# Optimization experiments

Measured on AMD Instinct MI355X. Metric: run time of the kernel, lower is better.

Reference implementation:

```python
import jax, jax.numpy as jnp
import numpy as np

B, S, H, L, NH, F, V = 8, 512, 768, 12, 12, 3072, 21128
DH = H // NH
SEP = 102
NEG = -1e9  # eager BERT additive mask: (1-mask)*large_negative


def _ln(x, g, b, eps=1e-12):
    m = jnp.mean(x, axis=-1, keepdims=True)
    v = jnp.var(x, axis=-1, keepdims=True)
    return (x - m) * jax.lax.rsqrt(v + eps) * g + b


def _mask_bias(input_ids):
    # prefix-LM mask: tokens <= first SEP fully bidirectional; suffix causal + sees prefix
    hit = input_ids == SEP                      # [B,S]
    has_sep = jnp.any(hit, axis=1)              # [B]
    first = jnp.argmax(hit, axis=1)             # [B] (first SEP position)
    sep = jnp.minimum(first, S - 2)             # clamp as in torch code
    pos = jnp.arange(S)
    i = pos[None, :, None]
    j = pos[None, None, :]
    sb = sep[:, None, None]
    vis = (j <= sb) | ((i > sb) & (j <= i))     # [B,S,S]
    vis = jnp.where(has_sep[:, None, None], vis, True)  # no SEP -> full ones
    return jnp.where(vis, 0.0, NEG).astype(jnp.float32)[:, None]  # [B,1,S,S]


def setup_inputs():
    key = jax.random.key(0)
    ks = jax.random.split(key, 4)
    input_ids = jax.random.randint(ks[0], (B, S), 0, V)
    sep_pos = jax.random.randint(ks[1], (B,), 32, 128)
    input_ids = input_ids.at[jnp.arange(B), sep_pos].set(SEP)
    labels = jax.random.randint(ks[2], (B, S), 0, V)
    pk = jax.random.split(ks[3], 10)
    n = lambda k, sh: jax.random.normal(k, sh, jnp.float32) * 0.02
    return dict(
        input_ids=input_ids, labels=labels,
        word_emb=n(pk[0], (V, H)), pos_emb=n(pk[1], (S, H)), type_emb=n(pk[2], (2, H)),
        emb_g=jnp.ones((H,), jnp.float32), emb_b=jnp.zeros((H,), jnp.float32),
        Wq=n(pk[3], (L, H, H)), bq=jnp.zeros((L, H), jnp.float32),
        Wk=n(pk[4], (L, H, H)), bk=jnp.zeros((L, H), jnp.float32),
        Wv=n(pk[5], (L, H, H)), bv=jnp.zeros((L, H), jnp.float32),
        Wo=n(pk[6], (L, H, H)), bo=jnp.zeros((L, H), jnp.float32),
        ln1_g=jnp.ones((L, H), jnp.float32), ln1_b=jnp.zeros((L, H), jnp.float32),
        W1=n(pk[7], (L, H, F)), b1=jnp.zeros((L, F), jnp.float32),
        W2=n(pk[8], (L, F, H)), b2=jnp.zeros((L, H), jnp.float32),
        ln2_g=jnp.ones((L, H), jnp.float32), ln2_b=jnp.zeros((L, H), jnp.float32),
        cls_W=n(pk[9], (H, V)), cls_b=jnp.zeros((V,), jnp.float32),
    )


def reference(input_ids, labels, word_emb, pos_emb, type_emb, emb_g, emb_b,
              Wq, bq, Wk, bk, Wv, bv, Wo, bo, ln1_g, ln1_b,
              W1, b1, W2, b2, ln2_g, ln2_b, cls_W, cls_b):
    bias = _mask_bias(input_ids)                               # [B,1,S,S]
    x = word_emb[input_ids] + pos_emb[None, :S] + type_emb[0]  # [B,S,H]
    x = _ln(x, emb_g, emb_b)

    def layer(h, p):
        wq, bq_, wk, bk_, wv, bv_, wo, bo_, g1, g1b, w1, bb1, w2, bb2, g2, g2b = p
        heads = lambda t: t.reshape(B, S, NH, DH).transpose(0, 2, 1, 3)
        q = heads(h @ wq + bq_)
        k = heads(h @ wk + bk_)
        v = heads(h @ wv + bv_)
        scores = jnp.einsum('bhqd,bhkd->bhqk', q, k) / np.sqrt(DH).astype(np.float32) + bias
        probs = jax.nn.softmax(scores, axis=-1)
        ctx = jnp.einsum('bhqk,bhkd->bhqd', probs, v).transpose(0, 2, 1, 3).reshape(B, S, H)
        h = _ln(h + ctx @ wo + bo_, g1, g1b)
        ffn = jax.nn.gelu(h @ w1 + bb1, approximate=False) @ w2 + bb2
        h = _ln(h + ffn, g2, g2b)
        return h, None

    x, _ = jax.lax.scan(layer, x, (Wq, bq, Wk, bk, Wv, bv, Wo, bo,
                                   ln1_g, ln1_b, W1, b1, W2, b2, ln2_g, ln2_b))
    logits = x @ cls_W + cls_b                                 # [B,S,V]

    # per-sample CE: mean over tokens after first SEP; full-sequence CE if no SEP
    logp = jax.nn.log_softmax(logits, axis=-1)
    ce = -jnp.take_along_axis(logp, labels[..., None], axis=-1)[..., 0]  # [B,S]
    hit = input_ids == SEP
    has_sep = jnp.any(hit, axis=1)
    first = jnp.argmax(hit, axis=1)
    pos = jnp.arange(S)[None]
    m = jnp.where(has_sep[:, None], pos > first[:, None], True).astype(ce.dtype)
    per_sample = jnp.sum(ce * m, axis=1) / jnp.sum(m, axis=1)
    return jnp.mean(per_sample)
```

## Files before the change

kernel.cpp:

```cpp
#include <hip/hip_runtime.h>
#include <math.h>

typedef unsigned short ushort;
typedef __bf16 bf16x8 __attribute__((ext_vector_type(8)));
typedef float f32x4 __attribute__((ext_vector_type(4)));

constexpr int Bb  = 8;
constexpr int Ss  = 512;
constexpr int Hh  = 768;
constexpr int Ll  = 12;
constexpr int NHh = 12;
constexpr int Ff  = 3072;
constexpr int Vv  = 21128;
constexpr int DHh = 64;
constexpr int Mm  = Bb * Ss;
constexpr int SEP_ID = 102;
constexpr int VP  = 21504;
constexpr int NCH = 24;
constexpr int TPC = 7;
constexpr int QKVN = 3 * Hh;
constexpr float LSE_SHIFT = 20.0f;

static __device__ __forceinline__ ushort f2bf(float f) {
    unsigned u = __float_as_uint(f);
    unsigned r = (u + 0x7fffu + ((u >> 16) & 1u)) >> 16;
    return (ushort)r;
}
static __device__ __forceinline__ float bf2f(unsigned x) {
    return __uint_as_float(x << 16);
}

__global__ __launch_bounds__(512) void sep_kernel(const int* __restrict__ ids,
                                                  int* __restrict__ info)
{
    int b = blockIdx.x;
    int t = threadIdx.x;
    int v = (ids[b * Ss + t] == SEP_ID) ? t : 0x7FFFFFFF;
    #pragma unroll
    for (int off = 32; off; off >>= 1) {
        int o = __shfl_xor(v, off);
        v = min(v, o);
    }
    __shared__ int wmin[8];
    int lane = t & 63, wid = t >> 6;
    if (lane == 0) wmin[wid] = v;
    __syncthreads();
    if (t == 0) {
        int first = wmin[0];
        #pragma unroll
        for (int w = 1; w < 8; w++) first = min(first, wmin[w]);
        int has = (first != 0x7FFFFFFF) ? 1 : 0;
        info[b * 4 + 0] = first;
        info[b * 4 + 1] = has;
        info[b * 4 + 2] = has ? min(first, Ss - 2) : (Ss + 1);
    }
}

__global__ __launch_bounds__(256) void embed_ln_kernel(
    const int* __restrict__ ids, const float* __restrict__ we,
    const float* __restrict__ pe, const float* __restrict__ te,
    const float* __restrict__ g, const float* __restrict__ bp,
    float* __restrict__ x, ushort* __restrict__ xb)
{
    int tok = blockIdx.x;
    int s = tok & (Ss - 1);
    int tid = threadIdx.x;
    int id = ids[tok];
    float e[3];
    #pragma unroll
    for (int r = 0; r < 3; r++) {
        int h = tid + (r << 8);
        e[r] = we[(size_t)id * Hh + h] + pe[(size_t)s * Hh + h] + te[h];
    }
    float sum = e[0] + e[1] + e[2];
    float sq  = fmaf(e[0], e[0], fmaf(e[1], e[1], e[2] * e[2]));
    #pragma unroll
    for (int off = 32; off; off >>= 1) {
        sum += __shfl_xor(sum, off);
        sq  += __shfl_xor(sq, off);
    }
    __shared__ float red[8];
    int lane = tid & 63, wid = tid >> 6;
    if (lane == 0) { red[wid] = sum; red[4 + wid] = sq; }
    __syncthreads();
    sum = red[0] + red[1] + red[2] + red[3];
    sq  = red[4] + red[5] + red[6] + red[7];
    float mean = sum * (1.0f / Hh);
    float var  = sq * (1.0f / Hh) - mean * mean;
    float rstd = rsqrtf(var + 1e-12f);
    #pragma unroll
    for (int r = 0; r < 3; r++) {
        int h = tid + (r << 8);
        float v = (e[r] - mean) * rstd * g[h] + bp[h];
        x[(size_t)tok * Hh + h] = v;
        xb[(size_t)tok * Hh + h] = f2bf(v);
    }
}

__global__ __launch_bounds__(256) void resid_ln_kernel(
    const float* __restrict__ resid, const float* __restrict__ y,
    const float* __restrict__ g, const float* __restrict__ bp,
    float* __restrict__ out, ushort* __restrict__ outb)
{
    int tok = blockIdx.x;
    int tid = threadIdx.x;
    float e[3];
    #pragma unroll
    for (int r = 0; r < 3; r++) {
        int h = tid + (r << 8);
        size_t idx = (size_t)tok * Hh + h;
        e[r] = resid[idx] + y[idx];
    }
    float sum = e[0] + e[1] + e[2];
    float sq  = fmaf(e[0], e[0], fmaf(e[1], e[1], e[2] * e[2]));
    #pragma unroll
    for (int off = 32; off; off >>= 1) {
        sum += __shfl_xor(sum, off);
        sq  += __shfl_xor(sq, off);
    }
    __shared__ float red[8];
    int lane = tid & 63, wid = tid >> 6;
    if (lane == 0) { red[wid] = sum; red[4 + wid] = sq; }
    __syncthreads();
    sum = red[0] + red[1] + red[2] + red[3];
    sq  = red[4] + red[5] + red[6] + red[7];
    float mean = sum * (1.0f / Hh);
    float var  = sq * (1.0f / Hh) - mean * mean;
    float rstd = rsqrtf(var + 1e-12f);
    #pragma unroll
    for (int r = 0; r < 3; r++) {
        int h = tid + (r << 8);
        float v = (e[r] - mean) * rstd * g[h] + bp[h];
        out[(size_t)tok * Hh + h] = v;
        outb[(size_t)tok * Hh + h] = f2bf(v);
    }
}

__global__ __launch_bounds__(256) void resid_ln4_kernel(
    const float* __restrict__ resid, const float* __restrict__ p,
    const float* __restrict__ bias, const float* __restrict__ g,
    const float* __restrict__ bp,
    float* __restrict__ out, ushort* __restrict__ outb)
{
    const size_t MHl = (size_t)Mm * Hh;
    int tok = blockIdx.x;
    int tid = threadIdx.x;
    float e[3];
    #pragma unroll
    for (int r = 0; r < 3; r++) {
        int h = tid + (r << 8);
        size_t idx = (size_t)tok * Hh + h;
        float acc = resid[idx] + bias[h];
        acc += p[idx];
        acc += p[MHl + idx];
        acc += p[2 * MHl + idx];
        acc += p[3 * MHl + idx];
        e[r] = acc;
    }
    float sum = e[0] + e[1] + e[2];
    float sq  = fmaf(e[0], e[0], fmaf(e[1], e[1], e[2] * e[2]));
    #pragma unroll
    for (int off = 32; off; off >>= 1) {
        sum += __shfl_xor(sum, off);
        sq  += __shfl_xor(sq, off);
    }
    __shared__ float red[8];
    int lane = tid & 63, wid = tid >> 6;
    if (lane == 0) { red[wid] = sum; red[4 + wid] = sq; }
    __syncthreads();
    sum = red[0] + red[1] + red[2] + red[3];
    sq  = red[4] + red[5] + red[6] + red[7];
    float mean = sum * (1.0f / Hh);
    float var  = sq * (1.0f / Hh) - mean * mean;
    float rstd = rsqrtf(var + 1e-12f);
    #pragma unroll
    for (int r = 0; r < 3; r++) {
        int h = tid + (r << 8);
        float v = (e[r] - mean) * rstd * g[h] + bp[h];
        out[(size_t)tok * Hh + h] = v;
        outb[(size_t)tok * Hh + h] = f2bf(v);
    }
}

__global__ __launch_bounds__(256) void prep_kernel(
    const float* __restrict__ Wq, const float* __restrict__ Wk,
    const float* __restrict__ Wv, const float* __restrict__ Wo,
    const float* __restrict__ W1, const float* __restrict__ W2,
    const float* __restrict__ bq, const float* __restrict__ bk,
    const float* __restrict__ bv,
    ushort* __restrict__ qkvoT, ushort* __restrict__ w1T,
    ushort* __restrict__ w2T, float* __restrict__ bqkv)
{
    int b = blockIdx.x;
    if (b >= 6912) {
        for (int j = threadIdx.x; j < Hh; j += 256) {
            bqkv[j]          = bq[j];
            bqkv[Hh + j]     = bk[j];
            bqkv[2 * Hh + j] = bv[j];
        }
        return;
    }
    const float* W;
    ushort* Wt;
    int K, N, n0, k0;
    if (b < 2304) {
        int which = b / 576, t = b % 576;
        const float* srcs[4] = { Wq, Wk, Wv, Wo };
        W = srcs[which];
        Wt = qkvoT + (size_t)which * Hh * Hh;
        K = Hh; N = Hh;
        n0 = (t % 24) * 32; k0 = (t / 24) * 32;
    } else if (b < 4608) {
        int t = b - 2304;
        W = W1; Wt = w1T; K = Hh; N = Ff;
        n0 = (t % 96) * 32; k0 = (t / 96) * 32;
    } else {
        int t = b - 4608;
        W = W2; Wt = w2T; K = Ff; N = Hh;
        n0 = (t % 24) * 32; k0 = (t / 24) * 32;
    }
    __shared__ float ts[32][33];
    int tx = threadIdx.x & 31, ty = threadIdx.x >> 5;
    #pragma unroll
    for (int i = 0; i < 32; i += 8)
        ts[ty + i][tx] = W[(size_t)(k0 + ty + i) * N + n0 + tx];
    __syncthreads();
    #pragma unroll
    for (int i = 0; i < 32; i += 8)
        Wt[(size_t)(n0 + ty + i) * K + k0 + tx] = f2bf(ts[tx][ty + i]);
}

__global__ __launch_bounds__(256) void pad_transpose_kernel(
    const float* __restrict__ W, ushort* __restrict__ Wt, int K, int N)
{
    __shared__ float ts[32][33];
    int n0 = blockIdx.x * 32, k0 = blockIdx.y * 32;
    int tx = threadIdx.x & 31, ty = threadIdx.x >> 5;
    #pragma unroll
    for (int i = 0; i < 32; i += 8) {
        int n = n0 + tx;
        ts[ty + i][tx] = (n < N) ? W[(size_t)(k0 + ty + i) * N + n] : 0.f;
    }
    __syncthreads();
    #pragma unroll
    for (int i = 0; i < 32; i += 8)
        Wt[(size_t)(n0 + ty + i) * K + k0 + tx] = f2bf(ts[tx][ty + i]);
}

__global__ __launch_bounds__(256) void bias_pad_kernel(
    const float* __restrict__ cb, float* __restrict__ cbp)
{
    int i = blockIdx.x * 256 + threadIdx.x;
    if (i < VP) cbp[i] = (i < Vv) ? cb[i] : -1.0e9f;
}

template <int ACT, int OUT_BF, int BIAS>
__global__ __launch_bounds__(256) void mfma_gemm(
    const ushort* __restrict__ A,
    const ushort* __restrict__ Bt,
    const float* __restrict__ bias,
    void* __restrict__ C,
    int N, int K, int lda, int ldb)
{
    __shared__ __align__(16) ushort As[128 * 32];
    __shared__ __align__(16) ushort Bs[128 * 32];
    const int tid = threadIdx.x;
    const int lane = tid & 63, wid = tid >> 6;
    const int m0 = blockIdx.y * 128, n0 = blockIdx.x * 128;
    const int kbase = blockIdx.z * K;
    const size_t zoff = (size_t)blockIdx.z * Mm * N;
    A += kbase;
    Bt += kbase;
    const int wr = (wid >> 1) * 64, wc = (wid & 1) * 64;
    const int lr = lane & 15;
    const int kg = (lane >> 4) << 3;

    f32x4 acc[4][4];
    #pragma unroll
    for (int mi = 0; mi < 4; ++mi)
        #pragma unroll
        for (int ni = 0; ni < 4; ++ni)
            acc[mi][ni] = (f32x4){0.f, 0.f, 0.f, 0.f};

    for (int k0 = 0; k0 < K; k0 += 32) {
        #pragma unroll
        for (int i = 0; i < 2; ++i) {
            int idx = i * 256 + tid;
            int r = idx >> 2, c = (idx & 3) << 3;
            __builtin_amdgcn_global_load_lds(
                (const __attribute__((address_space(1))) void*)(A + (size_t)(m0 + r) * lda + k0 + c),
                (__attribute__((address_space(3))) void*)(As + (size_t)(i * 256 + (wid << 6)) * 8),
                16, 0, 0);
        }
        #pragma unroll
        for (int i = 0; i < 2; ++i) {
            int idx = i * 256 + tid;
            int r = idx >> 2, c = (idx & 3) << 3;
            __builtin_amdgcn_global_load_lds(
                (const __attribute__((address_space(1))) void*)(Bt + (size_t)(n0 + r) * ldb + k0 + c),
                (__attribute__((address_space(3))) void*)(Bs + (size_t)(i * 256 + (wid << 6)) * 8),
                16, 0, 0);
        }
        __syncthreads();

        bf16x8 af[4], bfr[4];
        #pragma unroll
        for (int mi = 0; mi < 4; ++mi)
            af[mi] = *(const bf16x8*)(As + (size_t)(wr + mi * 16 + lr) * 32 + kg);
        #pragma unroll
        for (int ni = 0; ni < 4; ++ni)
            bfr[ni] = *(const bf16x8*)(Bs + (size_t)(wc + ni * 16 + lr) * 32 + kg);

        #pragma unroll
        for (int mi = 0; mi < 4; ++mi)
            #pragma unroll
            for (int ni = 0; ni < 4; ++ni)
                acc[mi][ni] = __builtin_amdgcn_mfma_f32_16x16x32_bf16(
                    af[mi], bfr[ni], acc[mi][ni], 0, 0, 0);
        __syncthreads();
    }

    #pragma unroll
    for (int ni = 0; ni < 4; ++ni) {
        int col = n0 + wc + ni * 16 + lr;
        float bsv = 0.f;
        if (BIAS) bsv = bias[col];
        #pragma unroll
        for (int mi = 0; mi < 4; ++mi) {
            f32x4 v = acc[mi][ni];
            #pragma unroll
            for (int q = 0; q < 4; ++q) {
                int row = m0 + wr + mi * 16 + ((lane >> 4) << 2) + q;
                float val = v[q] + bsv;
                if (ACT == 1) {
                    float y = 0.7978845608028654f
                              * (val + 0.044715f * val * val * val);
                    val = val / (1.0f + __expf(-2.0f * y));
                }
                if (OUT_BF)
                    ((ushort*)C)[(size_t)row * N + col] = f2bf(val);
                else
                    ((float*)C)[zoff + (size_t)row * N + col] = val;
            }
        }
    }
}

constexpr int SP = 65;
constexpr int PS = 72;
constexpr int VS = 72;

__global__ __launch_bounds__(256) void flash_attn_kernel(
    const ushort* __restrict__ qkv, const int* __restrict__ info,
    ushort* __restrict__ ctx)
{
    __shared__ __align__(16) ushort K_lds[64 * VS];
    __shared__ __align__(16) ushort Vt_lds[64 * VS];
    __shared__ __align__(16) ushort P_lds[64 * PS];
    __shared__ float S_lds[64 * SP];
    __shared__ float m_s[64], l_s[64], rf_s[64];

    const int tid = threadIdx.x;
    const int lane = tid & 63, wid = tid >> 6;
    const int bh = blockIdx.y, b = bh / NHh, h = bh % NHh;
    const int i0 = blockIdx.x * 64;
    const int lr = lane & 15, hi = lane >> 4;
    const int kg = hi << 3;
    const int wr = (wid >> 1) * 32;
    const int wc = (wid & 1) * 32;
    const int has = info[b * 4 + 1], sep = info[b * 4 + 2];
    const size_t tok0 = (size_t)b * Ss;

    bf16x8 qf[2][2];
    #pragma unroll
    for (int mi = 0; mi < 2; ++mi)
        #pragma unroll
        for (int kk = 0; kk < 2; ++kk)
            qf[mi][kk] = *(const bf16x8*)&qkv[(tok0 + i0 + wr + mi * 16 + lr) * QKVN
                                             + h * DHh + kk * 32 + kg];

    f32x4 o[2][2];
    #pragma unroll
    for (int mi = 0; mi < 2; ++mi)
        #pragma unroll
        for (int ni = 0; ni < 2; ++ni)
            o[mi][ni] = (f32x4){0.f, 0.f, 0.f, 0.f};

    if (tid < 64) { m_s[tid] = -3.0e38f; l_s[tid] = 0.f; }
    __syncthreads();

    for (int j0 = 0; j0 < Ss; j0 += 64) {
        #pragma unroll
        for (int i = 0; i < 2; ++i) {
            int ix = i * 256 + tid;
            int r = ix >> 3, c = (ix & 7) << 3;
            uint4 kq = *(const uint4*)&qkv[(tok0 + j0 + r) * QKVN + Hh + h * DHh + c];
            *(uint4*)&K_lds[(size_t)r * VS + c] = kq;
        }
        {
            int kv0 = (tid & 15) * 4;
            int d0 = (tid >> 4) * 4;
            uint2 rv[4];
            #pragma unroll
            for (int r = 0; r < 4; ++r)
                rv[r] = *(const uint2*)&qkv[(tok0 + j0 + kv0 + r) * QKVN
                                            + 2 * Hh + h * DHh + d0];
            #pragma unroll
            for (int c = 0; c < 4; ++c) {
                unsigned e0 = (c < 2) ? (rv[0].x >> (16 * c)) : (rv[0].y >> (16 * (c - 2)));
                unsigned e1 = (c < 2) ? (rv[1].x >> (16 * c)) : (rv[1].y >> (16 * (c - 2)));
                unsigned e2 = (c < 2) ? (rv[2].x >> (16 * c)) : (rv[2].y >> (16 * (c - 2)));
                unsigned e3 = (c < 2) ? (rv[3].x >> (16 * c)) : (rv[3].y >> (16 * (c - 2)));
                uint2 packed;
                packed.x = (e0 & 0xffffu) | (e1 << 16);
                packed.y = (e2 & 0xffffu) | (e3 << 16);
                *(uint2*)&Vt_lds[(size_t)(d0 + c) * VS + kv0] = packed;
            }
        }
        __syncthreads();

        f32x4 s[2][2];
        #pragma unroll
        for (int mi = 0; mi < 2; ++mi)
            #pragma unroll
            for (int ni = 0; ni < 2; ++ni)
                s[mi][ni] = (f32x4){0.f, 0.f, 0.f, 0.f};
        #pragma unroll
        for (int ni = 0; ni < 2; ++ni)
            #pragma unroll
            for (int kk = 0; kk < 2; ++kk) {
                bf16x8 kf = *(const bf16x8*)&K_lds[(size_t)(wc + ni * 16 + lr) * VS
                                                   + kk * 32 + kg];
                #pragma unroll
                for (int mi = 0; mi < 2; ++mi)
                    s[mi][ni] = __builtin_amdgcn_mfma_f32_16x16x32_bf16(
                        qf[mi][kk], kf, s[mi][ni], 0, 0, 0);
            }
        #pragma unroll
        for (int mi = 0; mi < 2; ++mi)
            #pragma unroll
            for (int ni = 0; ni < 2; ++ni)
                #pragma unroll
                for (int q = 0; q < 4; ++q) {
                    int rl = wr + mi * 16 + hi * 4 + q;
                    int cl = wc + ni * 16 + lr;
                    int gi = i0 + rl, gj = j0 + cl;
                    bool vis = (!has) || (gj <= sep) || ((gi > sep) && (gj <= gi));
                    S_lds[rl * SP + cl] = s[mi][ni][q] * 0.125f
                                          + (vis ? 0.0f : -1000000000.0f);
                }
        __syncthreads();

        {
            int r = tid >> 2, c0 = (tid & 3) * 16;
            float mold = m_s[r];
            float sv[16];
            float tmax = -3.0e38f;
            #pragma unroll
            for (int c = 0; c < 16; ++c) {
                sv[c] = S_lds[r * SP + c0 + c];
                tmax = fmaxf(tmax, sv[c]);
            }
            tmax = fmaxf(tmax, __shfl_xor(tmax, 1));
            tmax = fmaxf(tmax, __shfl_xor(tmax, 2));
            float mnew = fmaxf(mold, tmax);
            float sum = 0.f;
            #pragma unroll
            for (int c = 0; c < 16; ++c) {
                float p = __expf(sv[c] - mnew);
                P_lds[r * PS + c0 + c] = f2bf(p);
                sum += p;
            }
            sum += __shfl_xor(sum, 1);
            sum += __shfl_xor(sum, 2);
            if ((tid & 3) == 0) {
                float rf = __expf(mold - mnew);
                rf_s[r] = rf;
                l_s[r] = l_s[r] * rf + sum;
                m_s[r] = mnew;
            }
        }
        __syncthreads();

        #pragma unroll
        for (int mi = 0; mi < 2; ++mi)
            #pragma unroll
            for (int q = 0; q < 4; ++q) {
                float rf = rf_s[wr + mi * 16 + hi * 4 + q];
                #pragma unroll
                for (int ni = 0; ni < 2; ++ni)
                    o[mi][ni][q] *= rf;
            }
        #pragma unroll
        for (int kk = 0; kk < 2; ++kk) {
            bf16x8 pf[2];
            #pragma unroll
            for (int mi = 0; mi < 2; ++mi)
                pf[mi] = *(const bf16x8*)&P_lds[(size_t)(wr + mi * 16 + lr) * PS
                                                + kk * 32 + kg];
            #pragma unroll
            for (int ni = 0; ni < 2; ++ni) {
                bf16x8 vf = *(const bf16x8*)&Vt_lds[(size_t)(wc + ni * 16 + lr) * VS
                                                    + kk * 32 + kg];
                #pragma unroll
                for (int mi = 0; mi < 2; ++mi)
                    o[mi][ni] = __builtin_amdgcn_mfma_f32_16x16x32_bf16(
                        pf[mi], vf, o[mi][ni], 0, 0, 0);
            }
        }
        __syncthreads();
    }

    #pragma unroll
    for (int mi = 0; mi < 2; ++mi)
        #pragma unroll
        for (int q = 0; q < 4; ++q) {
            int rl = wr + mi * 16 + hi * 4 + q;
            float inv = 1.0f / l_s[rl];
            #pragma unroll
            for (int ni = 0; ni < 2; ++ni)
                ctx[(tok0 + i0 + rl) * Hh + h * DHh + wc + ni * 16 + lr]
                    = f2bf(o[mi][ni][q] * inv);
        }
}

__global__ __launch_bounds__(256) void cls_lse_kernel(
    const ushort* __restrict__ A,
    const ushort* __restrict__ WT,
    const float* __restrict__ cbp,
    const int* __restrict__ labels,
    float* __restrict__ psv, float* __restrict__ pll)
{
    __shared__ __align__(16) ushort As[128 * 32];
    __shared__ __align__(16) ushort Bs[128 * 32];
    __shared__ float ssum[2][128];
    __shared__ float sll[128];
    __shared__ int lab[128];
    const int tid = threadIdx.x;
    const int lane = tid & 63, wid = tid >> 6;
    const int m0 = blockIdx.y * 128;
    const int chunk = blockIdx.x;
    if (tid < 128) {
        sll[tid] = 0.f;
        lab[tid] = labels[m0 + tid];
    }
    const int wr = (wid >> 1) * 64, wcid = wid & 1, wc = wcid * 64;
    const int lr = lane & 15;
    const int hi = lane >> 4;
    const int kg = hi << 3;

    float sacc[16];
    #pragma unroll
    for (int i = 0; i < 16; ++i) sacc[i] = 0.f;

    for (int t = 0; t < TPC; ++t) {
        const int n0 = (chunk * TPC + t) * 128;
        f32x4 acc[4][4];
        #pragma unroll
        for (int mi = 0; mi < 4; ++mi)
            #pragma unroll
            for (int ni = 0; ni < 4; ++ni)
                acc[mi][ni] = (f32x4){0.f, 0.f, 0.f, 0.f};

        for (int k0 = 0; k0 < Hh; k0 += 32) {
            #pragma unroll
            for (int i = 0; i < 2; ++i) {
                int idx = i * 256 + tid;
                int r = idx >> 2, c = (idx & 3) << 3;
                __builtin_amdgcn_global_load_lds(
                    (const __attribute__((address_space(1))) void*)(A + (size_t)(m0 + r) * Hh + k0 + c),
                    (__attribute__((address_space(3))) void*)(As + (size_t)(i * 256 + (wid << 6)) * 8),
                    16, 0, 0);
            }
            #pragma unroll
            for (int i = 0; i < 2; ++i) {
                int idx = i * 256 + tid;
                int r = idx >> 2, c = (idx & 3) << 3;
                __builtin_amdgcn_global_load_lds(
                    (const __attribute__((address_space(1))) void*)(WT + (size_t)(n0 + r) * Hh + k0 + c),
                    (__attribute__((address_space(3))) void*)(Bs + (size_t)(i * 256 + (wid << 6)) * 8),
                    16, 0, 0);
            }
            __syncthreads();

            bf16x8 af[4], bfr[4];
            #pragma unroll
            for (int mi = 0; mi < 4; ++mi)
                af[mi] = *(const bf16x8*)(As + (size_t)(wr + mi * 16 + lr) * 32 + kg);
            #pragma unroll
            for (int ni = 0; ni < 4; ++ni)
                bfr[ni] = *(const bf16x8*)(Bs + (size_t)(wc + ni * 16 + lr) * 32 + kg);

            #pragma unroll
            for (int mi = 0; mi < 4; ++mi)
                #pragma unroll
                for (int ni = 0; ni < 4; ++ni)
                    acc[mi][ni] = __builtin_amdgcn_mfma_f32_16x16x32_bf16(
                        af[mi], bfr[ni], acc[mi][ni], 0, 0, 0);
            __syncthreads();
        }

        float bvs[4];
        int cols[4];
        #pragma unroll
        for (int ni = 0; ni < 4; ++ni) {
            cols[ni] = n0 + wc + ni * 16 + lr;
            bvs[ni] = cbp[cols[ni]];
        }
        #pragma unroll
        for (int mi = 0; mi < 4; ++mi) {
            #pragma unroll
            for (int q = 0; q < 4; ++q) {
                int rl = wr + mi * 16 + hi * 4 + q;
                float v0 = acc[mi][0][q] + bvs[0];
                float v1 = acc[mi][1][q] + bvs[1];
                float v2 = acc[mi][2][q] + bvs[2];
                float v3 = acc[mi][3][q] + bvs[3];
                int lb = lab[rl];
                if (lb == cols[0]) sll[rl] = v0;
                if (lb == cols[1]) sll[rl] = v1;
                if (lb == cols[2]) sll[rl] = v2;
                if (lb == cols[3]) sll[rl] = v3;
                sacc[mi * 4 + q] += __expf(v0 - LSE_SHIFT) + __expf(v1 - LSE_SHIFT)
                                  + __expf(v2 - LSE_SHIFT) + __expf(v3 - LSE_SHIFT);
            }
        }
    }

    #pragma unroll
    for (int mi = 0; mi < 4; ++mi) {
        #pragma unroll
        for (int q = 0; q < 4; ++q) {
            float s = sacc[mi * 4 + q];
            s += __shfl_xor(s, 1);
            s += __shfl_xor(s, 2);
            s += __shfl_xor(s, 4);
            s += __shfl_xor(s, 8);
            if (lr == 0) ssum[wcid][wr + mi * 16 + hi * 4 + q] = s;
        }
    }
    __syncthreads();
    if (tid < 128) {
        psv[(size_t)chunk * Mm + m0 + tid] = ssum[0][tid] + ssum[1][tid];
        pll[(size_t)chunk * Mm + m0 + tid] = sll[tid];
    }
}

__global__ __launch_bounds__(256) void cls_merge_kernel(
    const float* __restrict__ psv, const float* __restrict__ pll,
    float* __restrict__ ce)
{
    int row = blockIdx.x * 256 + threadIdx.x;
    float s = 0.f, l = 0.f;
    #pragma unroll 1
    for (int c = 0; c < NCH; ++c) {
        s += psv[(size_t)c * Mm + row];
        l += pll[(size_t)c * Mm + row];
    }
    ce[row] = (LSE_SHIFT + logf(s)) - l;
}

__global__ __launch_bounds__(256) void ce_reduce_kernel(
    const float* __restrict__ ce, const int* __restrict__ info,
    float* __restrict__ ps)
{
    int b = blockIdx.x, tid = threadIdx.x;
    int first = info[b * 4 + 0], has = info[b * 4 + 1];
    float sum = 0.0f;
    for (int s = tid; s < Ss; s += 256) {
        bool mv = has ? (s > first) : true;
        if (mv) sum += ce[b * Ss + s];
    }
    #pragma unroll
    for (int off = 32; off; off >>= 1) sum += __shfl_xor(sum, off);
    __shared__ float red[4];
    int lane = tid & 63, wid = tid >> 6;
    if (lane == 0) red[wid] = sum;
    __syncthreads();
    if (tid == 0) {
        float tot = red[0] + red[1] + red[2] + red[3];
        float cnt = has ? (float)(Ss - 1 - first) : (float)Ss;
        ps[b] = tot / cnt;
    }
}

__global__ void final_kernel(const float* __restrict__ ps, float* __restrict__ out)
{
    if (threadIdx.x == 0 && blockIdx.x == 0) {
        float t = 0.0f;
        #pragma unroll
        for (int b = 0; b < Bb; b++) t += ps[b];
        out[0] = t * (1.0f / Bb);
    }
}

extern "C" void kernel_launch(void* const* d_in, const int* in_sizes, int n_in,
                              void* d_out, int out_size, void* d_ws, size_t ws_size,
                              hipStream_t stream)
{
    const int*   ids    = (const int*)d_in[0];
    const int*   labels = (const int*)d_in[1];
    const float* we     = (const float*)d_in[2];
    const float* pe     = (const float*)d_in[3];
    const float* te     = (const float*)d_in[4];
    const float* eg     = (const float*)d_in[5];
    const float* ebp    = (const float*)d_in[6];
    const float* Wq     = (const float*)d_in[7];
    const float* bq     = (const float*)d_in[8];
    const float* Wk     = (const float*)d_in[9];
    const float* bk     = (const float*)d_in[10];
    const float* Wv     = (const float*)d_in[11];
    const float* bv     = (const float*)d_in[12];
    const float* Wo     = (const float*)d_in[13];
    const float* bo     = (const float*)d_in[14];
    const float* l1g    = (const float*)d_in[15];
    const float* l1b    = (const float*)d_in[16];
    const float* W1     = (const float*)d_in[17];
    const float* b1     = (const float*)d_in[18];
    const float* W2     = (const float*)d_in[19];
    const float* b2     = (const float*)d_in[20];
    const float* l2g    = (const float*)d_in[21];
    const float* l2b    = (const float*)d_in[22];
    const float* cW     = (const float*)d_in[23];
    const float* cbias  = (const float*)d_in[24];

    const size_t MH  = (size_t)Mm * Hh;
    const size_t MF  = (size_t)Mm * Ff;
    const size_t HHe = (size_t)Hh * Hh;
    const size_t HFe = (size_t)Hh * Ff;

    float* ws = (float*)d_ws;
    float* x      = ws;
    float* tmp    = x + MH;
    float* ce     = tmp + 4 * MH;
    float* ps     = ce + Mm;
    int*   info   = (int*)(ps + 16);
    float* bqkv   = (float*)(info + 64);
    ushort* xb    = (ushort*)(bqkv + QKVN);
    ushort* qkvb  = xb + MH;
    ushort* ctxb  = qkvb + 3 * MH;
    ushort* f1b   = ctxb + MH;
    ushort* wscr  = f1b + MF;
    ushort* wqT = wscr;
    ushort* woT = wqT + 3 * HHe;
    ushort* w1T = wscr + 4 * HHe;
    ushort* w2T = w1T + HFe;
    float* clsf = (float*)(w2T + HFe);
    float* cbp  = clsf;
    float* psv  = cbp + VP;
    float* pll  = psv + (size_t)NCH * Mm;
    ushort* cWT = qkvb;

    sep_kernel<<<Bb, 512, 0, stream>>>(ids, info);
    embed_ln_kernel<<<Mm, 256, 0, stream>>>(ids, we, pe, te, eg, ebp, x, xb);

    dim3 gQKV(QKVN / 128, Mm / 128);
    dim3 gH(Hh / 128, Mm / 128);
    dim3 gF(Ff / 128, Mm / 128);
    dim3 gW2(Hh / 128, Mm / 128, 4);
    dim3 gA(Ss / 64, Bb * NHh);

    for (int l = 0; l < Ll; l++) {
        const float* bo_l = bo + (size_t)l * Hh;
        const float* b1_l = b1 + (size_t)l * Ff;
        const float* b2_l = b2 + (size_t)l * Hh;
        const float* g1  = l1g + (size_t)l * Hh;
        const float* be1 = l1b + (size_t)l * Hh;
        const float* g2  = l2g + (size_t)l * Hh;
        const float* be2 = l2b + (size_t)l * Hh;

        prep_kernel<<<6913, 256, 0, stream>>>(
            Wq + (size_t)l * HHe, Wk + (size_t)l * HHe,
            Wv + (size_t)l * HHe, Wo + (size_t)l * HHe,
            W1 + (size_t)l * HFe, W2 + (size_t)l * HFe,
            bq + (size_t)l * Hh, bk + (size_t)l * Hh, bv + (size_t)l * Hh,
            wscr, w1T, w2T, bqkv);

        mfma_gemm<0, 1, 1><<<gQKV, 256, 0, stream>>>(xb, wqT, bqkv, qkvb,
                                                     QKVN, Hh, Hh, Hh);

        flash_attn_kernel<<<gA, 256, 0, stream>>>(qkvb, info, ctxb);

        mfma_gemm<0, 0, 1><<<gH, 256, 0, stream>>>(ctxb, woT, bo_l, tmp,
                                                   Hh, Hh, Hh, Hh);
        resid_ln_kernel<<<Mm, 256, 0, stream>>>(x, tmp, g1, be1, x, xb);

        mfma_gemm<1, 1, 1><<<gF, 256, 0, stream>>>(xb, w1T, b1_l, f1b,
                                                   Ff, Hh, Hh, Hh);
        mfma_gemm<0, 0, 0><<<gW2, 256, 0, stream>>>(f1b, w2T, nullptr, tmp,
                                                    Hh, Hh , Ff, Ff);
        resid_ln4_kernel<<<Mm, 256, 0, stream>>>(x, tmp, b2_l, g2, be2, x, xb);
    }

    pad_transpose_kernel<<<dim3(VP / 32, Hh / 32), 256, 0, stream>>>(cW, cWT, Hh, Vv);
    bias_pad_kernel<<<(VP + 255) / 256, 256, 0, stream>>>(cbias, cbp);
    cls_lse_kernel<<<dim3(NCH, Mm / 128), 256, 0, stream>>>(
        xb, cWT, cbp, labels, psv, pll);
    cls_merge_kernel<<<Mm / 256, 256, 0, stream>>>(psv, pll, ce);
    ce_reduce_kernel<<<Bb, 256, 0, stream>>>(ce, info, ps);
    final_kernel<<<1, 64, 0, stream>>>(ps, (float*)d_out);
}
```

Before: 2.620 ms.

## Split-K the attention output GEMM, rebalance classifier chunks, fuse CE merge/reduce

The Wo projection GEMM now runs split-K over 4 z-slices, writing partial sums that the existing resid_ln4 kernel adds together with the bias. This raises the grid from 192 to 768 blocks so the small 768x768 GEMM fills more compute units, at the cost of extra partial-sum memory traffic. The classifier LSE is split into 42 chunks of 4 tiles instead of 24 of 7, to improve load balance across the GPU. The CE merge and per-sample reduce kernels are fused into one launch, dropping the intermediate ce buffer.

```diff
diff --git a/kernel.cpp b/kernel.cpp
--- a/kernel.cpp
+++ b/kernel.cpp
@@ -16,8 +16,8 @@
 constexpr int Mm  = Bb * Ss;
 constexpr int SEP_ID = 102;
 constexpr int VP  = 21504;
-constexpr int NCH = 24;
-constexpr int TPC = 7;
+constexpr int NCH = 42;
+constexpr int TPC = 4;
 constexpr int QKVN = 3 * Hh;
 constexpr float LSE_SHIFT = 20.0f;
 
@@ -94,45 +94,6 @@
         float v = (e[r] - mean) * rstd * g[h] + bp[h];
         x[(size_t)tok * Hh + h] = v;
         xb[(size_t)tok * Hh + h] = f2bf(v);
-    }
-}
-
-__global__ __launch_bounds__(256) void resid_ln_kernel(
-    const float* __restrict__ resid, const float* __restrict__ y,
-    const float* __restrict__ g, const float* __restrict__ bp,
-    float* __restrict__ out, ushort* __restrict__ outb)
-{
-    int tok = blockIdx.x;
-    int tid = threadIdx.x;
-    float e[3];
-    #pragma unroll
-    for (int r = 0; r < 3; r++) {
-        int h = tid + (r << 8);
-        size_t idx = (size_t)tok * Hh + h;
-        e[r] = resid[idx] + y[idx];
-    }
-    float sum = e[0] + e[1] + e[2];
-    float sq  = fmaf(e[0], e[0], fmaf(e[1], e[1], e[2] * e[2]));
-    #pragma unroll
-    for (int off = 32; off; off >>= 1) {
-        sum += __shfl_xor(sum, off);
-        sq  += __shfl_xor(sq, off);
-    }
-    __shared__ float red[8];
-    int lane = tid & 63, wid = tid >> 6;
-    if (lane == 0) { red[wid] = sum; red[4 + wid] = sq; }
-    __syncthreads();
-    sum = red[0] + red[1] + red[2] + red[3];
-    sq  = red[4] + red[5] + red[6] + red[7];
-    float mean = sum * (1.0f / Hh);
-    float var  = sq * (1.0f / Hh) - mean * mean;
-    float rstd = rsqrtf(var + 1e-12f);
-    #pragma unroll
-    for (int r = 0; r < 3; r++) {
-        int h = tid + (r << 8);
-        float v = (e[r] - mean) * rstd * g[h] + bp[h];
-        out[(size_t)tok * Hh + h] = v;
-        outb[(size_t)tok * Hh + h] = f2bf(v);
     }
 }
 
@@ -646,30 +607,26 @@
     }
 }
 
-__global__ __launch_bounds__(256) void cls_merge_kernel(
+__global__ __launch_bounds__(256) void cls_finish_kernel(
     const float* __restrict__ psv, const float* __restrict__ pll,
-    float* __restrict__ ce)
-{
-    int row = blockIdx.x * 256 + threadIdx.x;
-    float s = 0.f, l = 0.f;
-    #pragma unroll 1
-    for (int c = 0; c < NCH; ++c) {
-        s += psv[(size_t)c * Mm + row];
-        l += pll[(size_t)c * Mm + row];
-    }
-    ce[row] = (LSE_SHIFT + logf(s)) - l;
-}
-
-__global__ __launch_bounds__(256) void ce_reduce_kernel(
-    const float* __restrict__ ce, const int* __restrict__ info,
-    float* __restrict__ ps)
+    const int* __restrict__ info, float* __restrict__ ps)
 {
     int b = blockIdx.x, tid = threadIdx.x;
     int first = info[b * 4 + 0], has = info[b * 4 + 1];
-    float sum = 0.0f;
-    for (int s = tid; s < Ss; s += 256) {
+    float sum = 0.f;
+    #pragma unroll
+    for (int rr = 0; rr < 2; ++rr) {
+        int s = tid + rr * 256;
+        int row = b * Ss + s;
+        float sv = 0.f, l = 0.f;
+        #pragma unroll 1
+        for (int c = 0; c < NCH; ++c) {
+            sv += psv[(size_t)c * Mm + row];
+            l  += pll[(size_t)c * Mm + row];
+        }
+        float cev = (LSE_SHIFT + logf(sv)) - l;
         bool mv = has ? (s > first) : true;
-        if (mv) sum += ce[b * Ss + s];
+        if (mv) sum += cev;
     }
     #pragma unroll
     for (int off = 32; off; off >>= 1) sum += __shfl_xor(sum, off);
@@ -732,8 +689,7 @@
     float* ws = (float*)d_ws;
     float* x      = ws;
     float* tmp    = x + MH;
-    float* ce     = tmp + 4 * MH;
-    float* ps     = ce + Mm;
+    float* ps     = tmp + 4 * MH;
     int*   info   = (int*)(ps + 16);
     float* bqkv   = (float*)(info + 64);
     ushort* xb    = (ushort*)(bqkv + QKVN);
@@ -755,7 +711,7 @@
     embed_ln_kernel<<<Mm, 256, 0, stream>>>(ids, we, pe, te, eg, ebp, x, xb);
 
     dim3 gQKV(QKVN / 128, Mm / 128);
-    dim3 gH(Hh / 128, Mm / 128);
+    dim3 gWo(Hh / 128, Mm / 128, 4);
     dim3 gF(Ff / 128, Mm / 128);
     dim3 gW2(Hh / 128, Mm / 128, 4);
     dim3 gA(Ss / 64, Bb * NHh);
@@ -781,9 +737,9 @@
 
         flash_attn_kernel<<<gA, 256, 0, stream>>>(qkvb, info, ctxb);
 
-        mfma_gemm<0, 0, 1><<<gH, 256, 0, stream>>>(ctxb, woT, bo_l, tmp,
-                                                   Hh, Hh, Hh, Hh);
-        resid_ln_kernel<<<Mm, 256, 0, stream>>>(x, tmp, g1, be1, x, xb);
+        mfma_gemm<0, 0, 0><<<gWo, 256, 0, stream>>>(ctxb, woT, nullptr, tmp,
+                                                    Hh, Hh / 4, Hh, Hh);
+        resid_ln4_kernel<<<Mm, 256, 0, stream>>>(x, tmp, bo_l, g1, be1, x, xb);
 
         mfma_gemm<1, 1, 1><<<gF, 256, 0, stream>>>(xb, w1T, b1_l, f1b,
                                                    Ff, Hh, Hh, Hh);
@@ -796,7 +752,6 @@
     bias_pad_kernel<<<(VP + 255) / 256, 256, 0, stream>>>(cbias, cbp);
     cls_lse_kernel<<<dim3(NCH, Mm / 128), 256, 0, stream>>>(
         xb, cWT, cbp, labels, psv, pll);
-    cls_merge_kernel<<<Mm / 256, 256, 0, stream>>>(psv, pll, ce);
-    ce_reduce_kernel<<<Bb, 256, 0, stream>>>(ce, info, ps);
+    cls_finish_kernel<<<Bb, 256, 0, stream>>>(psv, pll, info, ps);
     final_kernel<<<1, 64, 0, stream>>>(ps, (float*)d_out);
 }
```

Result: no change. 2.608 ms (-0.5%).
